# Kernel tuning notes

Hardware: AMD Instinct MI355X
Metric: run time of the kernel (lower is better)

## Reference

```python
import jax, jax.numpy as jnp
import numpy as np

D_MODEL = 1024
ED = 2048          # d_inner = 2 * d_model
N = 16             # d_state
DT_RANK = 64
K = 4              # d_conv
BETA = 0.6
ALPHA = 1.0
B_SZ, L = 1, 2048


def setup_inputs() -> dict:
    key = jax.random.key(0)
    ks = jax.random.split(key, 9)
    s = 0.02
    x = jax.random.normal(ks[0], (B_SZ, L, D_MODEL), jnp.float32)
    W_in = jax.random.normal(ks[1], (2 * ED, D_MODEL), jnp.float32) * s
    conv_w = jax.random.normal(ks[2], (ED, K), jnp.float32) * s
    conv_b = jax.random.normal(ks[3], (ED,), jnp.float32) * s
    W_x = jax.random.normal(ks[4], (DT_RANK + 2 * N, ED), jnp.float32) * s
    dt_std = DT_RANK ** -0.5
    W_dt = jax.random.uniform(ks[5], (ED, DT_RANK), jnp.float32, -dt_std, dt_std)
    # dt bias init: inverse-softplus of dt in [dt_min, dt_max]
    dt = jnp.exp(jax.random.uniform(ks[6], (ED,), jnp.float32)
                 * (np.log(0.1) - np.log(0.001)) + np.log(0.001))
    dt = jnp.clip(dt, 1e-4)
    b_dt = dt + jnp.log(-jnp.expm1(-dt))
    A_log = jnp.log(jnp.tile(jnp.arange(1, N + 1, dtype=jnp.float32), (ED, 1)))
    D = jnp.ones((ED,), jnp.float32)
    W_out = jax.random.normal(ks[7], (D_MODEL, ED), jnp.float32) * s
    return {"x": x, "W_in": W_in, "conv_w": conv_w, "conv_b": conv_b,
            "W_x": W_x, "W_dt": W_dt, "b_dt": b_dt, "A_log": A_log,
            "D": D, "W_out": W_out}


def _depthwise_causal_conv(xc, conv_w, conv_b):
    # xc: (B, L, ED); torch Conv1d(groups=ED, padding=K-1)[..., :L] == causal conv
    lhs = jnp.transpose(xc, (0, 2, 1))                       # (B, ED, L)
    lhs = jnp.pad(lhs, ((0, 0), (0, 0), (K - 1, 0)))
    out = jax.lax.conv_general_dilated(lhs, conv_w[:, None, :], (1,), 'VALID',
                                       feature_group_count=ED)  # (B, ED, L)
    return jnp.transpose(out, (0, 2, 1)) + conv_b


def _ssm_momentum(xc, W_x, W_dt, b_dt, A_log, D):
    A = -jnp.exp(A_log)                                      # (ED, N)
    dBC = xc @ W_x.T                                         # (B, L, dt_rank + 2N)
    delta, Bm, Cm = jnp.split(dBC, [DT_RANK, DT_RANK + N], axis=-1)
    delta = jax.nn.softplus(delta @ W_dt.T + b_dt)           # (B, L, ED)
    deltaA = jnp.exp(delta[..., None] * A)                   # (B, L, ED, N)
    u = ALPHA * delta[..., None] * Bm[:, :, None, :] * xc[..., None]  # (B, L, ED, N)

    def step(carry, inp):
        h, v = carry
        dA_t, u_t = inp
        v = BETA * v + u_t
        h = dA_t * h + v
        return (h, v), h

    h0 = jnp.zeros((xc.shape[0], ED, N), xc.dtype)
    _, hs = jax.lax.scan(step, (h0, h0),
                         (jnp.moveaxis(deltaA, 1, 0), jnp.moveaxis(u, 1, 0)))
    y = jnp.einsum('lben,bln->ble', hs, Cm)                  # (B, L, ED)
    return y + D * xc


def reference(x, W_in, conv_w, conv_b, W_x, W_dt, b_dt, A_log, D, W_out):
    xz = x @ W_in.T                                          # (B, L, 2*ED)
    xc, z = jnp.split(xz, 2, axis=-1)
    xc = jax.nn.silu(_depthwise_causal_conv(xc, conv_w, conv_b))
    y = _ssm_momentum(xc, W_x, W_dt, b_dt, A_log, D)
    return (y * jax.nn.silu(z)) @ W_out.T                    # (B, L, d_model)
```

## Files before the change

kernel.cpp:

```cpp
#include <hip/hip_runtime.h>
#include <hip/hip_bf16.h>
#include <math.h>

#define L 2048
#define DM 1024
#define ED 2048
#define NST 16
#define DTR 64
#define BETA 0.6f
#define NCHUNK 64
#define LCH 32
#define SPLITS 32
#define SPLIT4 4

typedef __bf16 bf16_t;
typedef __bf16 bf16x8 __attribute__((ext_vector_type(8)));
typedef __bf16 bf16x4 __attribute__((ext_vector_type(4)));
typedef __bf16 bf16x2 __attribute__((ext_vector_type(2)));
typedef float  floatx4 __attribute__((ext_vector_type(4)));


__global__ void k_fill(float* __restrict__ p, float v, int n) {
    int i = blockIdx.x * 256 + threadIdx.x;
    if (i < n) p[i] = v;
}

__global__ void k_cvt_all(const float4* __restrict__ s0, bf16x4* __restrict__ d0,
                          const float4* __restrict__ s1, bf16x4* __restrict__ d1,
                          const float4* __restrict__ s2, bf16x4* __restrict__ d2,
                          const float4* __restrict__ s3, bf16x4* __restrict__ d3,
                          const float4* __restrict__ s4, bf16x4* __restrict__ d4) {
    int i = blockIdx.x * 256 + threadIdx.x;
    const float4* s; bf16x4* d; int j;
    if (i < 524288)        { s = s0; d = d0; j = i; }
    else if (i < 1572864)  { s = s1; d = d1; j = i - 524288; }
    else if (i < 1622016)  { s = s2; d = d2; j = i - 1572864; }
    else if (i < 1654784)  { s = s3; d = d3; j = i - 1622016; }
    else                   { s = s4; d = d4; j = i - 1654784; }
    float4 f = s[j];
    bf16x4 o;
    o[0] = (bf16_t)f.x; o[1] = (bf16_t)f.y; o[2] = (bf16_t)f.z; o[3] = (bf16_t)f.w;
    d[j] = o;
}

template<int EPI, bool GUARD>
__global__ __launch_bounds__(256)
void k_gemm_bt(const bf16_t* __restrict__ X, int lda,
               const bf16_t* __restrict__ W,
               float* __restrict__ C, int M, int N, int K, int ldc, int ksz,
               const float* __restrict__ bias,
               const float* __restrict__ cw, const float* __restrict__ cb) {
    constexpr int BK = GUARD ? 32 : 64;
    constexpr int NB = GUARD ? 1 : 2;
    __shared__ bf16_t As[NB][128 * BK];
    __shared__ bf16_t Bs[NB][128 * BK];
    const int tid  = threadIdx.x;
    const int bx   = blockIdx.x, by = blockIdx.y;
    const int kbase = blockIdx.z * ksz;
    const size_t zoff = (size_t)blockIdx.z * M * ldc;
    const int wave = tid >> 6, lane = tid & 63;
    const int wm   = (wave >> 1) * 64;
    const int wn   = (wave & 1) * 64;
    const int quad = lane >> 4, l16 = lane & 15;

    floatx4 acc[4][4];
#pragma unroll
    for (int i = 0; i < 4; i++)
#pragma unroll
        for (int j = 0; j < 4; j++)
            acc[i][j] = (floatx4){0.f, 0.f, 0.f, 0.f};

    if (!GUARD) {
        auto stage = [&](int buf, int kt) {
#pragma unroll
            for (int p = 0; p < 4; p++) {
                int e = p * 2048 + tid * 8;
                int r = e >> 6, c = e & 63;
                int cs = c ^ ((r & 7) << 3);
                __builtin_amdgcn_global_load_lds(
                    (const __attribute__((address_space(1))) void*)&X[(size_t)(by * 128 + r) * lda + kt + cs],
                    (__attribute__((address_space(3))) void*)&As[buf][e], 16, 0, 0);
                __builtin_amdgcn_global_load_lds(
                    (const __attribute__((address_space(1))) void*)&W[(size_t)(bx * 128 + r) * K + kt + cs],
                    (__attribute__((address_space(3))) void*)&Bs[buf][e], 16, 0, 0);
            }
        };
        stage(0, kbase);
        __syncthreads();
        int cur = 0;
        for (int kt = kbase; kt < kbase + ksz; kt += 64) {
            if (kt + 64 < kbase + ksz) stage(cur ^ 1, kt + 64);
#pragma unroll
            for (int ks = 0; ks < 2; ks++) {
                bf16x8 af[4], bfr[4];
#pragma unroll
                for (int mt = 0; mt < 4; mt++) {
                    int R = wm + mt * 16 + l16;
                    af[mt] = *(const bf16x8*)(&As[cur][R * 64 + ((ks * 32 + quad * 8) ^ ((R & 7) << 3))]);
                }
#pragma unroll
                for (int nt = 0; nt < 4; nt++) {
                    int R = wn + nt * 16 + l16;
                    bfr[nt] = *(const bf16x8*)(&Bs[cur][R * 64 + ((ks * 32 + quad * 8) ^ ((R & 7) << 3))]);
                }
#pragma unroll
                for (int mt = 0; mt < 4; mt++)
#pragma unroll
                    for (int nt = 0; nt < 4; nt++)
                        acc[mt][nt] = __builtin_amdgcn_mfma_f32_16x16x32_bf16(
                            af[mt], bfr[nt], acc[mt][nt], 0, 0, 0);
            }
            __syncthreads();
            cur ^= 1;
        }
    } else {
        for (int kt = kbase; kt < kbase + ksz; kt += 32) {
#pragma unroll
            for (int p = 0; p < 2; p++) {
                int e = p * 2048 + tid * 8;
                int r = e >> 5, c = e & 31;
                int t   = by * 128 + r;
                int col = kt + c;
                float accv[8];
#pragma unroll
                for (int j = 0; j < 8; j++) accv[j] = cb[col + j];
                float4 wj[8];
#pragma unroll
                for (int j = 0; j < 8; j++)
                    wj[j] = *(const float4*)(&cw[(col + j) * 4]);
#pragma unroll
                for (int k = 0; k < 4; k++) {
                    int tt = t - 3 + k;
                    if (tt >= 0) {
                        bf16x8 xv = *(const bf16x8*)(&X[(size_t)tt * lda + col]);
#pragma unroll
                        for (int j = 0; j < 8; j++)
                            accv[j] += ((const float*)&wj[j])[k] * (float)xv[j];
                    }
                }
                bf16x8 av;
#pragma unroll
                for (int j = 0; j < 8; j++) {
                    float s = accv[j] / (1.f + __expf(-accv[j]));
                    av[j] = (bf16_t)s;
                }
                *(bf16x8*)(&As[0][r * 32 + c]) = av;
                int brow = bx * 128 + r;
                float4 bv = make_float4(0.f, 0.f, 0.f, 0.f);
                if (brow < N) bv = *(const float4*)(&W[(size_t)brow * K + kt + c]);
                *(float4*)(&Bs[0][r * 32 + c]) = bv;
            }
            __syncthreads();

            bf16x8 af[4], bfr[4];
#pragma unroll
            for (int mt = 0; mt < 4; mt++)
                af[mt] = *(const bf16x8*)(&As[0][(wm + mt * 16 + l16) * 32 + quad * 8]);
#pragma unroll
            for (int nt = 0; nt < 4; nt++)
                bfr[nt] = *(const bf16x8*)(&Bs[0][(wn + nt * 16 + l16) * 32 + quad * 8]);
#pragma unroll
            for (int mt = 0; mt < 4; mt++)
#pragma unroll
                for (int nt = 0; nt < 4; nt++)
                    acc[mt][nt] = __builtin_amdgcn_mfma_f32_16x16x32_bf16(
                        af[mt], bfr[nt], acc[mt][nt], 0, 0, 0);
            __syncthreads();
        }
    }

#pragma unroll
    for (int mt = 0; mt < 4; mt++) {
#pragma unroll
        for (int nt = 0; nt < 4; nt++) {
            int col = bx * 128 + wn + nt * 16 + l16;
            if (!GUARD || col < N) {
#pragma unroll
                for (int r4 = 0; r4 < 4; r4++) {
                    int row = by * 128 + wm + mt * 16 + quad * 4 + r4;
                    float v = acc[mt][nt][r4];
                    size_t off = zoff + (size_t)row * ldc + col;
                    if (EPI == 0) {
                        C[off] = v;
                    } else if (EPI == 1) {
                        v += bias[col];
                        v = (v > 20.f) ? v : __logf(1.f + __expf(v));
                        ((bf16_t*)C)[off] = (bf16_t)v;
                    } else {
                        ((bf16_t*)C)[off] = (bf16_t)v;
                    }
                }
            }
        }
    }
}

__global__ void k_red4(const bf16x8* __restrict__ part, float4* __restrict__ out) {
    int i = blockIdx.x * 256 + threadIdx.x;
    const int stride = L * DM / 8;
    bf16x8 a = part[i], b = part[i + stride];
    bf16x8 c = part[i + 2 * stride], d = part[i + 3 * stride];
    float4 o0, o1;
    o0.x = (float)a[0] + (float)b[0] + (float)c[0] + (float)d[0];
    o0.y = (float)a[1] + (float)b[1] + (float)c[1] + (float)d[1];
    o0.z = (float)a[2] + (float)b[2] + (float)c[2] + (float)d[2];
    o0.w = (float)a[3] + (float)b[3] + (float)c[3] + (float)d[3];
    o1.x = (float)a[4] + (float)b[4] + (float)c[4] + (float)d[4];
    o1.y = (float)a[5] + (float)b[5] + (float)c[5] + (float)d[5];
    o1.z = (float)a[6] + (float)b[6] + (float)c[6] + (float)d[6];
    o1.w = (float)a[7] + (float)b[7] + (float)c[7] + (float)d[7];
    out[2 * i]     = o0;
    out[2 * i + 1] = o1;
}

__global__ void k_red2(const float* __restrict__ part, float* __restrict__ dBC,
                       bf16_t* __restrict__ dly) {
    int idx = blockIdx.x * 256 + threadIdx.x;
    int t = idx / 96, c = idx - t * 96;
    float s = 0.f;
#pragma unroll
    for (int sp = 0; sp < SPLITS; sp++) s += part[(size_t)sp * L * 96 + idx];
    dBC[idx] = s;
    if (c < 64) dly[t * 64 + c] = (bf16_t)s;
}


__global__ __launch_bounds__(256)
void k_scan_p1(const bf16_t* __restrict__ delta, const bf16_t* __restrict__ xz,
               const float* __restrict__ conv_w, const float* __restrict__ conv_b,
               const float* __restrict__ dBC, const float* __restrict__ A_log,
               float2* __restrict__ hv, bf16x2* __restrict__ pq) {
    const int chunk = blockIdx.x >> 3;
    const int e = (blockIdx.x & 7) * 256 + threadIdx.x;
    float A[NST];
#pragma unroll
    for (int n = 0; n < NST; n++) A[n] = -__expf(A_log[e * NST + n]);
    float h[NST], v[NST], p[NST], q[NST];
#pragma unroll
    for (int n = 0; n < NST; n++) { h[n] = 0.f; v[n] = 0.f; p[n] = 1.f; q[n] = 0.f; }
    float bp = 1.f;
    const int t0 = chunk * LCH;
    const bf16_t* xzx = xz + e;
    const float4 wv = *(const float4*)(&conv_w[e * 4]);
    const float cbv = conv_b[e];
    float x0 = (t0 >= 3) ? (float)xzx[(size_t)(t0 - 3) * 4096] : 0.f;
    float x1 = (t0 >= 2) ? (float)xzx[(size_t)(t0 - 2) * 4096] : 0.f;
    float x2 = (t0 >= 1) ? (float)xzx[(size_t)(t0 - 1) * 4096] : 0.f;
    for (int i = 0; i < LCH; i++) {
        int t = t0 + i;
        float x3 = (float)xzx[(size_t)t * 4096];
        float a4 = cbv + wv.x * x0 + wv.y * x1 + wv.z * x2 + wv.w * x3;
        float xcv = a4 / (1.f + __expf(-a4));
        x0 = x1; x1 = x2; x2 = x3;
        float d   = (float)delta[(size_t)t * ED + e];
        float du  = d * xcv;
        bp *= BETA;
        const float* Bp = &dBC[t * 96 + 64];
#pragma unroll
        for (int n = 0; n < NST; n++) {
            float a = __expf(d * A[n]);
            v[n] = BETA * v[n] + du * Bp[n];
            h[n] = a * h[n] + v[n];
            p[n] *= a;
            q[n] = a * q[n] + bp;
        }
    }
#pragma unroll
    for (int n = 0; n < NST; n++) {
        size_t idx = ((size_t)n * NCHUNK + chunk) * ED + e;
        hv[idx] = make_float2(h[n], v[n]);
        bf16x2 z; z[0] = (bf16_t)p[n]; z[1] = (bf16_t)q[n];
        pq[idx] = z;
    }
}

__global__ void k_combine(float2* __restrict__ hv, const bf16x2* __restrict__ pq) {
    int tid = blockIdx.x * 256 + threadIdx.x;
    int n = tid >> 11, e = tid & (ED - 1);
    float h = 0.f, v = 0.f;
    const float bl = 7.9586611e-8f;
#pragma unroll 4
    for (int c = 0; c < NCHUNK; c++) {
        size_t idx = ((size_t)n * NCHUNK + c) * ED + e;
        float2 f = hv[idx];
        bf16x2 z = pq[idx];
        hv[idx] = make_float2(h, v);
        float hn = (float)z[0] * h + (float)z[1] * v + f.x;
        v = bl * v + f.y;
        h = hn;
    }
}

__global__ __launch_bounds__(256)
void k_scan_p2(const bf16_t* __restrict__ delta, const bf16_t* __restrict__ xz,
               const float* __restrict__ conv_w, const float* __restrict__ conv_b,
               const float* __restrict__ dBC, const float* __restrict__ A_log,
               const float2* __restrict__ hv, const float* __restrict__ Dvec,
               bf16_t* __restrict__ g) {
    const int chunk = blockIdx.x >> 3;
    const int e = (blockIdx.x & 7) * 256 + threadIdx.x;
    float A[NST];
#pragma unroll
    for (int n = 0; n < NST; n++) A[n] = -__expf(A_log[e * NST + n]);
    float h[NST], v[NST];
#pragma unroll
    for (int n = 0; n < NST; n++) {
        float2 s = hv[((size_t)n * NCHUNK + chunk) * ED + e];
        h[n] = s.x; v[n] = s.y;
    }
    const float De = Dvec[e];
    const int t0 = chunk * LCH;
    const bf16_t* xzx = xz + e;
    const float4 wv = *(const float4*)(&conv_w[e * 4]);
    const float cbv = conv_b[e];
    float x0 = (t0 >= 3) ? (float)xzx[(size_t)(t0 - 3) * 4096] : 0.f;
    float x1 = (t0 >= 2) ? (float)xzx[(size_t)(t0 - 2) * 4096] : 0.f;
    float x2 = (t0 >= 1) ? (float)xzx[(size_t)(t0 - 1) * 4096] : 0.f;
    for (int i = 0; i < LCH; i++) {
        int t = t0 + i;
        float x3 = (float)xzx[(size_t)t * 4096];
        float a4 = cbv + wv.x * x0 + wv.y * x1 + wv.z * x2 + wv.w * x3;
        float xcv = a4 / (1.f + __expf(-a4));
        x0 = x1; x1 = x2; x2 = x3;
        float d   = (float)delta[(size_t)t * ED + e];
        float du  = d * xcv;
        const float* Bp = &dBC[t * 96 + 64];
        const float* Cp = &dBC[t * 96 + 80];
        float yacc = 0.f;
#pragma unroll
        for (int n = 0; n < NST; n++) {
            float a = __expf(d * A[n]);
            v[n] = BETA * v[n] + du * Bp[n];
            h[n] = a * h[n] + v[n];
            yacc += Cp[n] * h[n];
        }
        float z = (float)xz[(size_t)t * 4096 + ED + e];
        float sz = z / (1.f + __expf(-z));
        g[(size_t)t * ED + e] = (bf16_t)((yacc + De * xcv) * sz);
    }
}


extern "C" void kernel_launch(void* const* d_in, const int* in_sizes, int n_in,
                              void* d_out, int out_size, void* d_ws, size_t ws_size,
                              hipStream_t stream) {
    const float* x      = (const float*)d_in[0];
    const float* W_in   = (const float*)d_in[1];
    const float* conv_w = (const float*)d_in[2];
    const float* conv_b = (const float*)d_in[3];
    const float* W_x    = (const float*)d_in[4];
    const float* W_dt   = (const float*)d_in[5];
    const float* b_dt   = (const float*)d_in[6];
    const float* A_log  = (const float*)d_in[7];
    const float* Dv     = (const float*)d_in[8];
    const float* W_out  = (const float*)d_in[9];
    float* out = (float*)d_out;

    constexpr size_t OFF_XZ    = 0;
    constexpr size_t OFF_XC    = 33554432;
    constexpr size_t OFF_C     = 50331648;
    constexpr size_t OFF_DELTA = 58720256;
    constexpr size_t OFF_R1    = 75497472;
    constexpr size_t OFF_XBF   = 109051904;
    constexpr size_t OFF_DBC   = 113246208;
    constexpr size_t OFF_DLY   = 114032640;
    constexpr size_t OFF_WX    = 114294784;
    constexpr size_t OFF_WDT   = 114688000;
    constexpr size_t OFF_WOUT  = 114950144;
    constexpr size_t WS_NEED   = 119144448;

    if (ws_size < WS_NEED) {
        k_fill<<<(out_size + 255) / 256, 256, 0, stream>>>(out, 1.0e9f, out_size);
        return;
    }

    char* ws = (char*)d_ws;
    bf16_t* xz_bf = (bf16_t*)(ws + OFF_XZ);
    bf16_t* part4 = (bf16_t*)(ws + OFF_XZ);
    float2* hv    = (float2*)(ws + OFF_XC);
    bf16_t* delta_bf = (bf16_t*)(ws + OFF_DELTA);
    bf16_t* g_bf  = (bf16_t*)(ws + OFF_DELTA + 8388608);
    bf16_t* Win_bf  = (bf16_t*)(ws + OFF_R1);
    float*  part2   = (float*)(ws + OFF_R1);
    bf16x2* pq      = (bf16x2*)(ws + OFF_R1);
    bf16_t* x_bf  = (bf16_t*)(ws + OFF_XBF);
    float*  dBC   = (float*)(ws + OFF_DBC);
    bf16_t* dly   = (bf16_t*)(ws + OFF_DLY);
    bf16_t* Wx_bf  = (bf16_t*)(ws + OFF_WX);
    bf16_t* Wdt_bf = (bf16_t*)(ws + OFF_WDT);
    bf16_t* Wout_bf = (bf16_t*)(ws + OFF_WOUT);

    k_cvt_all<<<8512, 256, 0, stream>>>(
        (const float4*)x,     (bf16x4*)x_bf,
        (const float4*)W_in,  (bf16x4*)Win_bf,
        (const float4*)W_x,   (bf16x4*)Wx_bf,
        (const float4*)W_dt,  (bf16x4*)Wdt_bf,
        (const float4*)W_out, (bf16x4*)Wout_bf);

    {
        dim3 g(4096 / 128, L / 128, 1);
        k_gemm_bt<2, false><<<g, 256, 0, stream>>>(
            x_bf, DM, Win_bf, (float*)xz_bf, L, 4096, DM, 4096, DM,
            nullptr, nullptr, nullptr);
    }
    {
        dim3 g(1, L / 128, SPLITS);
        k_gemm_bt<0, true><<<g, 256, 0, stream>>>(
            xz_bf, 4096, Wx_bf, part2, L, 96, ED, 96, ED / SPLITS,
            nullptr, conv_w, conv_b);
    }
    k_red2<<<L * 96 / 256, 256, 0, stream>>>(part2, dBC, dly);
    {
        dim3 g(ED / 128, L / 128, 1);
        k_gemm_bt<1, false><<<g, 256, 0, stream>>>(
            dly, DTR, Wdt_bf, (float*)delta_bf, L, ED, DTR, ED, DTR,
            b_dt, nullptr, nullptr);
    }
    k_scan_p1<<<NCHUNK * 8, 256, 0, stream>>>(delta_bf, xz_bf, conv_w, conv_b,
                                              dBC, A_log, hv, pq);
    k_combine<<<ED * NST / 256, 256, 0, stream>>>(hv, pq);
    k_scan_p2<<<NCHUNK * 8, 256, 0, stream>>>(delta_bf, xz_bf, conv_w, conv_b,
                                              dBC, A_log, hv, Dv, g_bf);
    {
        dim3 g(DM / 128, L / 128, SPLIT4);
        k_gemm_bt<2, false><<<g, 256, 0, stream>>>(
            g_bf, ED, Wout_bf, (float*)part4, L, DM, ED, DM, ED / SPLIT4,
            nullptr, nullptr, nullptr);
    }
    k_red4<<<L * DM / 8 / 256, 256, 0, stream>>>((const bf16x8*)part4, (float4*)out);
}
```

Baseline: 239.4 us.

## Parallelize chunk-combine scan across four lanes per chain with shuffle composition

The sequential 64-step cross-chunk combine per (n,e) chain is split across four threads, each handling 16 chunks. Each thread composes its segment's affine transform, and the segment prefixes are combined with wavefront shuffles before each thread rewrites its carried states. This targets the latency of a serial dependent chain in a small kernel with few threads. In exchange it issues four times as many threads, does extra arithmetic to compose the transforms, and changes the order of floating-point operations.

Result: no change. 238.5 us (-0.4%).

```diff
diff --git a/kernel.cpp b/kernel.cpp
--- a/kernel.cpp
+++ b/kernel.cpp
@@ -274,19 +274,51 @@
     }
 }
 
-__global__ void k_combine(float2* __restrict__ hv, const bf16x2* __restrict__ pq) {
-    int tid = blockIdx.x * 256 + threadIdx.x;
-    int n = tid >> 11, e = tid & (ED - 1);
-    float h = 0.f, v = 0.f;
+__global__ __launch_bounds__(256)
+void k_combine_par(float2* __restrict__ hv, const bf16x2* __restrict__ pq) {
     const float bl = 7.9586611e-8f;
-#pragma unroll 4
-    for (int c = 0; c < NCHUNK; c++) {
-        size_t idx = ((size_t)n * NCHUNK + c) * ED + e;
+    int w = blockIdx.x * 256 + threadIdx.x;
+    int chain = w >> 2, j = w & 3;
+    int cn = chain >> 11, ce = chain & (ED - 1);
+    float hl[16], vl[16], pp[16], qq[16];
+#pragma unroll
+    for (int i = 0; i < 16; i++) {
+        size_t idx = ((size_t)cn * NCHUNK + (j * 16 + i)) * ED + ce;
         float2 f = hv[idx];
         bf16x2 z = pq[idx];
+        hl[i] = f.x; vl[i] = f.y;
+        pp[i] = (float)z[0]; qq[i] = (float)z[1];
+    }
+    float P = 1.f, Q = 0.f, B = 1.f, H = 0.f, V = 0.f;
+#pragma unroll
+    for (int i = 0; i < 16; i++) {
+        float Hn = pp[i] * H + qq[i] * V + hl[i];
+        float Vn = bl * V + vl[i];
+        float Qn = pp[i] * Q + qq[i] * B;
+        float Pn = pp[i] * P;
+        float Bn = bl * B;
+        H = Hn; V = Vn; Q = Qn; P = Pn; B = Bn;
+    }
+    int lane = threadIdx.x & 63;
+    int base = lane & ~3;
+    float h = 0.f, v = 0.f;
+#pragma unroll
+    for (int k = 0; k < 3; k++) {
+        float Pk = __shfl(P, base + k), Qk = __shfl(Q, base + k);
+        float Bk = __shfl(B, base + k);
+        float Hk = __shfl(H, base + k), Vk = __shfl(V, base + k);
+        if (k < j) {
+            float hn = Pk * h + Qk * v + Hk;
+            v = Bk * v + Vk;
+            h = hn;
+        }
+    }
+#pragma unroll
+    for (int i = 0; i < 16; i++) {
+        size_t idx = ((size_t)cn * NCHUNK + (j * 16 + i)) * ED + ce;
         hv[idx] = make_float2(h, v);
-        float hn = (float)z[0] * h + (float)z[1] * v + f.x;
-        v = bl * v + f.y;
+        float hn = pp[i] * h + qq[i] * v + hl[i];
+        v = bl * v + vl[i];
         h = hn;
     }
 }
@@ -418,7 +450,7 @@
     }
     k_scan_p1<<<NCHUNK * 8, 256, 0, stream>>>(delta_bf, xz_bf, conv_w, conv_b,
                                               dBC, A_log, hv, pq);
-    k_combine<<<ED * NST / 256, 256, 0, stream>>>(hv, pq);
+    k_combine_par<<<ED * NST * 4 / 256, 256, 0, stream>>>(hv, pq);
     k_scan_p2<<<NCHUNK * 8, 256, 0, stream>>>(delta_bf, xz_bf, conv_w, conv_b,
                                               dBC, A_log, hv, Dv, g_bf);
     {
```
